# Kernel tuning notes

Hardware: AMD Instinct MI355X
Metric: run time of the kernel (lower is better)

## Reference

```python
import jax, jax.numpy as jnp
import numpy as np

N, E, F_IN = 100000, 600000, 128
HID, NCLS = 128, 2
# ratio=0.8 applied three times: ceil(0.8*100000), ceil(0.8*80000), ceil(0.8*64000)
K1, K2, K3 = 80000, 64000, 51200


def setup_inputs() -> dict:
    key = jax.random.key(0)
    k = jax.random.split(key, 16)
    s = 0.05
    p = {}
    p['x'] = jax.random.normal(k[0], (N, F_IN), dtype=jnp.float32)
    p['edge_index'] = jax.random.randint(k[1], (2, E), 0, N)
    # GraphConv i: out = lin_rel(sum_j x_j) + lin_root(x_i); lin_root has no bias (PyG)
    p['Wr1'] = jax.random.normal(k[2], (HID, F_IN), jnp.float32) * s
    p['br1'] = jnp.zeros((HID,), jnp.float32)
    p['Wroot1'] = jax.random.normal(k[3], (HID, F_IN), jnp.float32) * s
    p['pw1'] = jax.random.normal(k[4], (HID,), jnp.float32) * s
    p['Wr2'] = jax.random.normal(k[5], (HID, HID), jnp.float32) * s
    p['br2'] = jnp.zeros((HID,), jnp.float32)
    p['Wroot2'] = jax.random.normal(k[6], (HID, HID), jnp.float32) * s
    p['pw2'] = jax.random.normal(k[7], (HID,), jnp.float32) * s
    p['Wr3'] = jax.random.normal(k[8], (HID, HID), jnp.float32) * s
    p['br3'] = jnp.zeros((HID,), jnp.float32)
    p['Wroot3'] = jax.random.normal(k[9], (HID, HID), jnp.float32) * s
    p['pw3'] = jax.random.normal(k[10], (HID,), jnp.float32) * s
    p['W_lin1'] = jax.random.normal(k[11], (HID, 2 * HID), jnp.float32) * s
    p['b_lin1'] = jnp.zeros((HID,), jnp.float32)
    p['W_lin2'] = jax.random.normal(k[12], (64, HID), jnp.float32) * s
    p['b_lin2'] = jnp.zeros((64,), jnp.float32)
    p['W_lin3'] = jax.random.normal(k[13], (NCLS, 64), jnp.float32) * s
    p['b_lin3'] = jnp.zeros((NCLS,), jnp.float32)
    return p


def _gconv(x, src, dst, emask, Wr, br, Wroot):
    # PyG GraphConv(aggr='add'): masked edges contribute zero (== removed edge)
    msg = x[src] * emask[:, None].astype(x.dtype)           # [E, F]
    agg = jax.ops.segment_sum(msg, dst, num_segments=x.shape[0])
    return agg @ Wr.T + br + x @ Wroot.T


def _topk_pool(x, src, dst, emask, w, k):
    # PyG TopKPooling: score = tanh((x.w)/||w||); keep top-k nodes; x = x[perm]*score[perm]
    score = jnp.tanh((x @ w) / jnp.linalg.norm(w))
    vals, perm = jax.lax.top_k(score, k)
    x_new = x[perm] * vals[:, None]
    new_idx = jnp.full((x.shape[0],), -1, jnp.int32).at[perm].set(
        jnp.arange(k, dtype=jnp.int32))
    ns, nd = new_idx[src], new_idx[dst]
    valid = emask & (ns >= 0) & (nd >= 0)
    return x_new, jnp.where(valid, ns, 0), jnp.where(valid, nd, 0), valid


def _readout(x):
    # single graph (batch=None): gmp || gap -> [1, 2F]
    return jnp.concatenate([x.max(axis=0), x.mean(axis=0)])[None, :]


def reference(x, edge_index, Wr1, br1, Wroot1, pw1, Wr2, br2, Wroot2, pw2,
              Wr3, br3, Wroot3, pw3, W_lin1, b_lin1, W_lin2, b_lin2, W_lin3, b_lin3):
    src = edge_index[0].astype(jnp.int32)
    dst = edge_index[1].astype(jnp.int32)
    emask = jnp.ones((src.shape[0],), dtype=bool)

    h = jax.nn.relu(_gconv(x, src, dst, emask, Wr1, br1, Wroot1))
    h, src, dst, emask = _topk_pool(h, src, dst, emask, pw1, K1)
    r1 = _readout(h)

    h = jax.nn.relu(_gconv(h, src, dst, emask, Wr2, br2, Wroot2))
    h, src, dst, emask = _topk_pool(h, src, dst, emask, pw2, K2)
    r2 = _readout(h)

    h = jax.nn.relu(_gconv(h, src, dst, emask, Wr3, br3, Wroot3))
    h, src, dst, emask = _topk_pool(h, src, dst, emask, pw3, K3)
    r3 = _readout(h)

    z = r1 + r2 + r3                                        # [1, 256]
    z = jax.nn.relu(z @ W_lin1.T + b_lin1)                  # dropout: inference no-op
    z = jax.nn.relu(z @ W_lin2.T + b_lin2)
    return z @ W_lin3.T + b_lin3                            # [1, num_classes]
```

## Files before the change

kernel.cpp:

```cpp
#include <hip/hip_runtime.h>
#include <hip/hip_bf16.h>
#include <math.h>

#define N0 100000
#define E0 600000
#define KP1 80000
#define KP2 64000
#define KP3 51200
#define F 128
#define RPB 2048
#define RMID 128
#define SCAN_CHUNK 1024
#define NCHUNK ((N0 + SCAN_CHUNK - 1) / SCAN_CHUNK)

typedef __attribute__((ext_vector_type(8))) short short8;
typedef __attribute__((ext_vector_type(8))) unsigned short ushort8;
typedef __attribute__((ext_vector_type(4))) float f32x4;

__device__ __forceinline__ unsigned fkey(float f) {
    unsigned u = __float_as_uint(f);
    return u ^ ((u & 0x80000000u) ? 0xFFFFFFFFu : 0x80000000u);
}
__device__ __forceinline__ unsigned short f2b(float f) {
    __hip_bfloat16 h = __float2bfloat16(f);
    return *(unsigned short*)&h;
}
__device__ __forceinline__ float b2f(unsigned short u) {
    __hip_bfloat16 h;
    *(unsigned short*)&h = u;
    return __bfloat162float(h);
}

__global__ __launch_bounds__(256) void cvt4K(const float* __restrict__ in,
                                             unsigned short* __restrict__ out, int n4) {
    int i = blockIdx.x * 256 + threadIdx.x;
    if (i >= n4) return;
    float4 v = *(const float4*)(in + (size_t)i * 4);
    *(ushort4*)(out + (size_t)i * 4) = make_ushort4(f2b(v.x), f2b(v.y), f2b(v.z), f2b(v.w));
}

__global__ __launch_bounds__(256) void cvtWAllK(const float* __restrict__ a0, const float* __restrict__ a1,
                                                const float* __restrict__ a2, const float* __restrict__ a3,
                                                const float* __restrict__ a4, const float* __restrict__ a5,
                                                unsigned short* __restrict__ o) {
    int m = blockIdx.y;
    const float* src = (m == 0) ? a0 : (m == 1) ? a1 : (m == 2) ? a2 : (m == 3) ? a3 : (m == 4) ? a4 : a5;
    int i = blockIdx.x * 256 + threadIdx.x;
    float4 v = *(const float4*)(src + (size_t)i * 4);
    *(ushort4*)(o + (size_t)m * 16384 + (size_t)i * 4) = make_ushort4(f2b(v.x), f2b(v.y), f2b(v.z), f2b(v.w));
}

__global__ __launch_bounds__(128) void pwnK(const float* __restrict__ p0, const float* __restrict__ p1,
                                            const float* __restrict__ p2, float* __restrict__ pwn) {
    __shared__ float sh[128];
    int l = blockIdx.x, t = threadIdx.x;
    const float* p = (l == 0) ? p0 : (l == 1) ? p1 : p2;
    float v = p[t];
    sh[t] = v * v;
    __syncthreads();
    for (int off = 64; off; off >>= 1) {
        if (t < off) sh[t] += sh[t + off];
        __syncthreads();
    }
    pwn[l * 128 + t] = v / sqrtf(sh[0]);
}

__global__ __launch_bounds__(256) void histDstK(const int* __restrict__ dst, unsigned* __restrict__ cnt) {
    int e = blockIdx.x * 256 + threadIdx.x;
    if (e < E0) atomicAdd(&cnt[dst[e]], 1u);
}

__global__ __launch_bounds__(256) void scanReduceK(const unsigned* __restrict__ cnt,
                                                   unsigned* __restrict__ chunkSum, int nbins) {
    __shared__ unsigned sh[256];
    int base = blockIdx.x * SCAN_CHUNK + threadIdx.x * 4;
    unsigned s = 0;
#pragma unroll
    for (int i = 0; i < 4; i++) { int b = base + i; if (b < nbins) s += cnt[b]; }
    sh[threadIdx.x] = s;
    __syncthreads();
    for (int off = 128; off; off >>= 1) {
        if (threadIdx.x < off) sh[threadIdx.x] += sh[threadIdx.x + off];
        __syncthreads();
    }
    if (threadIdx.x == 0) chunkSum[blockIdx.x] = sh[0];
}

__global__ void scanChunksK(const unsigned* __restrict__ chunkSum, unsigned* __restrict__ chunkOff,
                            int nchunks, unsigned* __restrict__ totalOut) {
    if (threadIdx.x == 0) {
        unsigned run = 0;
        for (int i = 0; i < nchunks; i++) { chunkOff[i] = run; run += chunkSum[i]; }
        *totalOut = run;
    }
}

__global__ __launch_bounds__(256) void scanFinalK(const unsigned* __restrict__ cnt,
                                                  const unsigned* __restrict__ chunkOff,
                                                  unsigned* __restrict__ rowptr, int nbins) {
    __shared__ unsigned sh[256];
    int t = threadIdx.x;
    int base = blockIdx.x * SCAN_CHUNK + t * 4;
    unsigned c[4], s = 0;
#pragma unroll
    for (int i = 0; i < 4; i++) { int b = base + i; c[i] = (b < nbins) ? cnt[b] : 0u; s += c[i]; }
    sh[t] = s;
    __syncthreads();
    for (int off = 1; off < 256; off <<= 1) {
        unsigned v = (t >= off) ? sh[t - off] : 0u;
        __syncthreads();
        sh[t] += v;
        __syncthreads();
    }
    unsigned basep = chunkOff[blockIdx.x] + sh[t] - s;
#pragma unroll
    for (int i = 0; i < 4; i++) {
        int b = base + i;
        if (b < nbins) { rowptr[b] = basep; basep += c[i]; }
    }
}

__global__ __launch_bounds__(256) void scatterFillK(const int* __restrict__ src,
                                                    const int* __restrict__ dst,
                                                    const unsigned* __restrict__ rowptr,
                                                    unsigned* __restrict__ fill,
                                                    int* __restrict__ sortedSrc) {
    int e = blockIdx.x * 256 + threadIdx.x;
    if (e >= E0) return;
    int d = dst[e];
    unsigned p = rowptr[d] + atomicAdd(&fill[d], 1u);
    sortedSrc[p] = src[e];
}

__global__ __launch_bounds__(256) void iotaK(int* o, int n) {
    int i = blockIdx.x * 256 + threadIdx.x;
    if (i < n) o[i] = i;
}

__global__ __launch_bounds__(256) void aggSegB(const unsigned short* __restrict__ x,
                                               const int* __restrict__ srcCur,
                                               const unsigned* __restrict__ rowptr,
                                               const int* __restrict__ orig,
                                               unsigned short* __restrict__ agg, int n) {
    int g = blockIdx.x * 16 + (threadIdx.x >> 4);
    int q = threadIdx.x & 15;
    if (g >= n) return;
    int d = orig[g];
    unsigned e0 = rowptr[d], e1 = rowptr[d + 1];
    float a[8];
#pragma unroll
    for (int j = 0; j < 8; j++) a[j] = 0.f;
    unsigned e = e0;
    for (; e + 4 <= e1; e += 4) {
        int s0 = srcCur[e], s1 = srcCur[e + 1], s2 = srcCur[e + 2], s3 = srcCur[e + 3];
        ushort8 v0 = *(const ushort8*)(x + (size_t)(s0 < 0 ? 0 : s0) * F + q * 8);
        ushort8 v1 = *(const ushort8*)(x + (size_t)(s1 < 0 ? 0 : s1) * F + q * 8);
        ushort8 v2 = *(const ushort8*)(x + (size_t)(s2 < 0 ? 0 : s2) * F + q * 8);
        ushort8 v3 = *(const ushort8*)(x + (size_t)(s3 < 0 ? 0 : s3) * F + q * 8);
        float m0 = s0 < 0 ? 0.f : 1.f, m1 = s1 < 0 ? 0.f : 1.f;
        float m2 = s2 < 0 ? 0.f : 1.f, m3 = s3 < 0 ? 0.f : 1.f;
#pragma unroll
        for (int j = 0; j < 8; j++) {
            a[j] = fmaf(b2f(v0[j]), m0, a[j]);
            a[j] = fmaf(b2f(v1[j]), m1, a[j]);
            a[j] = fmaf(b2f(v2[j]), m2, a[j]);
            a[j] = fmaf(b2f(v3[j]), m3, a[j]);
        }
    }
    for (; e < e1; e++) {
        int s = srcCur[e];
        if (s < 0) continue;
        ushort8 v = *(const ushort8*)(x + (size_t)s * F + q * 8);
#pragma unroll
        for (int j = 0; j < 8; j++) a[j] += b2f(v[j]);
    }
    ushort8 o;
#pragma unroll
    for (int j = 0; j < 8; j++) o[j] = f2b(a[j]);
    *(ushort8*)(agg + (size_t)g * F + q * 8) = o;
}

__global__ __launch_bounds__(256) void buildOrigK(const int* __restrict__ origIn,
                                                  const int* __restrict__ nidx,
                                                  int* __restrict__ origOut, int n) {
    int i = blockIdx.x * 256 + threadIdx.x;
    if (i < n) { int ni = nidx[i]; if (ni >= 0) origOut[ni] = origIn[i]; }
}

__global__ __launch_bounds__(256) void remapSrcK(const int* __restrict__ srcIn,
                                                 const int* __restrict__ nidx,
                                                 int* __restrict__ srcOut) {
    int e = blockIdx.x * 256 + threadIdx.x;
    if (e >= E0) return;
    int s = srcIn[e];
    srcOut[e] = (s >= 0) ? nidx[s] : -1;
}

#define CPAD 40
__global__ __launch_bounds__(256) void convM(const unsigned short* __restrict__ A0,
                                             const unsigned short* __restrict__ A1,
                                             const unsigned short* __restrict__ W0,
                                             const unsigned short* __restrict__ W1,
                                             const float* __restrict__ br,
                                             const float* __restrict__ pwn,
                                             unsigned short* __restrict__ hbf,
                                             float* __restrict__ sc,
                                             unsigned* __restrict__ keys, int n) {
    __shared__ unsigned short As[128 * CPAD];
    __shared__ unsigned short Bs[128 * CPAD];
    int tid = threadIdx.x;
    int w = tid >> 6, l = tid & 63;
    int r = l & 15, g = l >> 4;
    int bm = blockIdx.x * 128;
    int srow = tid >> 2, q4 = tid & 3;

    f32x4 acc[2][8];
#pragma unroll
    for (int m = 0; m < 2; m++)
#pragma unroll
        for (int c = 0; c < 8; c++) acc[m][c] = (f32x4){0.f, 0.f, 0.f, 0.f};

    for (int ph = 0; ph < 2; ph++) {
        const unsigned short* A = ph ? A1 : A0;
        const unsigned short* W = ph ? W1 : W0;
        for (int kk = 0; kk < 128; kk += 32) {
            __syncthreads();
#pragma unroll
            for (int h2 = 0; h2 < 2; h2++) {
                int rr = srow + h2 * 64;
                uint4 av = make_uint4(0u, 0u, 0u, 0u);
                if (bm + rr < n) av = *(const uint4*)(A + (size_t)(bm + rr) * F + kk + q4 * 8);
                *(uint4*)(&As[rr * CPAD + q4 * 8]) = av;
                uint4 wv = *(const uint4*)(W + (size_t)rr * F + kk + q4 * 8);
                *(uint4*)(&Bs[rr * CPAD + q4 * 8]) = wv;
            }
            __syncthreads();
            short8 af[2], bf[8];
#pragma unroll
            for (int m = 0; m < 2; m++)
                af[m] = *(const short8*)(&As[(w * 32 + m * 16 + r) * CPAD + g * 8]);
#pragma unroll
            for (int c = 0; c < 8; c++)
                bf[c] = *(const short8*)(&Bs[(c * 16 + r) * CPAD + g * 8]);
#pragma unroll
            for (int m = 0; m < 2; m++)
#pragma unroll
                for (int c = 0; c < 8; c++)
                    acc[m][c] = __builtin_amdgcn_mfma_f32_16x16x32_bf16(af[m], bf[c], acc[m][c], 0, 0, 0);
        }
    }

    float pd[2][4];
#pragma unroll
    for (int m = 0; m < 2; m++)
#pragma unroll
        for (int j = 0; j < 4; j++) pd[m][j] = 0.f;

#pragma unroll
    for (int c = 0; c < 8; c++) {
        int col = c * 16 + r;
        float bias = br[col];
        float pwc = pwn[col];
#pragma unroll
        for (int m = 0; m < 2; m++) {
#pragma unroll
            for (int j = 0; j < 4; j++) {
                int row = bm + w * 32 + m * 16 + g * 4 + j;
                float h = fmaxf(acc[m][c][j] + bias, 0.f);
                pd[m][j] += h * pwc;
                if (row < n) hbf[(size_t)row * F + col] = f2b(h);
            }
        }
    }
#pragma unroll
    for (int m = 0; m < 2; m++) {
#pragma unroll
        for (int j = 0; j < 4; j++) {
            float p = pd[m][j];
            p += __shfl_xor(p, 1);
            p += __shfl_xor(p, 2);
            p += __shfl_xor(p, 4);
            p += __shfl_xor(p, 8);
            if (r == 0) {
                int row = bm + w * 32 + m * 16 + g * 4 + j;
                if (row < n) {
                    float s = tanhf(p);
                    sc[row] = s;
                    keys[row] = fkey(s);
                }
            }
        }
    }
}

__global__ void initSelK(unsigned* hist, unsigned* st, unsigned* done, unsigned* done2, int k) {
    hist[threadIdx.x] = 0;
    if (threadIdx.x == 0) { st[0] = 0u; st[1] = (unsigned)k; *done = 0u; *done2 = 0u; }
}

__global__ __launch_bounds__(256) void histSelK(const unsigned* __restrict__ keys, int n,
                                                int p, unsigned* __restrict__ st,
                                                unsigned* __restrict__ hist,
                                                unsigned* __restrict__ done, int nb) {
    __shared__ unsigned lh[256];
    __shared__ bool last;
    int tid = threadIdx.x;
    lh[tid] = 0;
    __syncthreads();
    unsigned prefix = st[0];
    int i = blockIdx.x * 256 + tid;
    if (i < n) {
        unsigned key = keys[i];
        bool m = (p == 0) || ((key >> (32 - 8 * p)) == (prefix >> (32 - 8 * p)));
        if (m) atomicAdd(&lh[(key >> (24 - 8 * p)) & 255u], 1u);
    }
    __syncthreads();
    if (lh[tid]) atomicAdd(&hist[tid], lh[tid]);
    __syncthreads();
    if (tid == 0) {
        __threadfence();
        last = (atomicAdd(done, 1u) == (unsigned)(nb - 1));
    }
    __syncthreads();
    if (!last) return;
    lh[tid] = atomicAdd(&hist[tid], 0u);
    __syncthreads();
    hist[tid] = 0;
    if (tid == 0) {
        unsigned krem = st[1], cum = 0;
        for (int b = 255; b >= 0; b--) {
            unsigned c = lh[b];
            if (cum + c >= krem) {
                st[0] |= ((unsigned)b) << (24 - 8 * p);
                st[1] = krem - cum;
                break;
            }
            cum += c;
        }
        *done = 0u;
    }
}

__global__ __launch_bounds__(256) void countsK(const unsigned* __restrict__ keys, int n,
                                               const unsigned* __restrict__ st,
                                               int* __restrict__ bGT, int* __restrict__ bEQ,
                                               int* __restrict__ sGT, int* __restrict__ sEQ,
                                               unsigned* __restrict__ done2, int nb) {
    __shared__ int cg_, ce_;
    __shared__ bool last;
    int tid = threadIdx.x;
    if (tid == 0) { cg_ = 0; ce_ = 0; }
    __syncthreads();
    unsigned t = st[0];
    int g = 0, e = 0;
    for (int it = 0; it < 4; it++) {
        int i = blockIdx.x * 1024 + it * 256 + tid;
        if (i < n) {
            unsigned k = keys[i];
            g += (k > t);
            e += (k == t);
        }
    }
    atomicAdd(&cg_, g);
    atomicAdd(&ce_, e);
    __syncthreads();
    if (tid == 0) {
        bGT[blockIdx.x] = cg_;
        bEQ[blockIdx.x] = ce_;
        __threadfence();
        last = (atomicAdd(done2, 1u) == (unsigned)(nb - 1));
    }
    __syncthreads();
    if (!last) return;
    if (tid == 0) {
        int gs = 0, es = 0;
        for (int b = 0; b < nb; b++) {
            sGT[b] = gs; sEQ[b] = es;
            gs += atomicAdd(&bGT[b], 0);
            es += atomicAdd(&bEQ[b], 0);
        }
        *done2 = 0u;
    }
}

__global__ __launch_bounds__(256) void markK(const unsigned* __restrict__ keys, int n,
                                             const unsigned* __restrict__ st,
                                             const int* __restrict__ sGT,
                                             const int* __restrict__ sEQ,
                                             int* __restrict__ nidx) {
    __shared__ int wG[4], wE[4];
    __shared__ int runG, runE;
    int tid = threadIdx.x, wv = tid >> 6, lane = tid & 63;
    if (tid == 0) { runG = 0; runE = 0; }
    unsigned t = st[0];
    int needEq = (int)st[1];
    int gOff = sGT[blockIdx.x], eOff = sEQ[blockIdx.x];
    unsigned long long mlt = (((unsigned long long)1) << lane) - 1ull;
    __syncthreads();
    for (int it = 0; it < 4; it++) {
        int i = blockIdx.x * 1024 + it * 256 + tid;
        bool inb = i < n;
        unsigned k = inb ? keys[i] : 0u;
        bool pG = inb && (k > t), pE = inb && (k == t);
        unsigned long long bG = __ballot(pG), bE = __ballot(pE);
        int lpG = __popcll(bG & mlt), lpE = __popcll(bE & mlt);
        if (lane == 0) { wG[wv] = __popcll(bG); wE[wv] = __popcll(bE); }
        __syncthreads();
        int woG = 0, woE = 0;
        for (int w = 0; w < wv; w++) { woG += wG[w]; woE += wE[w]; }
        int gB = gOff + runG + woG + lpG;
        int eB = eOff + runE + woE + lpE;
        int ni = -1;
        if (pG) ni = gB + (eB < needEq ? eB : needEq);
        else if (pE && eB < needEq) ni = gB + eB;
        if (inb) nidx[i] = ni;
        __syncthreads();
        if (tid == 0) {
            runG += wG[0] + wG[1] + wG[2] + wG[3];
            runE += wE[0] + wE[1] + wE[2] + wE[3];
        }
        __syncthreads();
    }
}

__global__ __launch_bounds__(256) void gatherB(const unsigned short* __restrict__ h,
                                               const float* __restrict__ sc,
                                               const int* __restrict__ nidx,
                                               unsigned short* __restrict__ out, int n) {
    int t = blockIdx.x * 256 + threadIdx.x;
    int i = t >> 4, q = t & 15;
    if (i >= n) return;
    int ni = nidx[i];
    if (ni < 0) return;
    float s = sc[i];
    ushort8 v = *(const ushort8*)(h + (size_t)i * F + q * 8);
    ushort8 o;
#pragma unroll
    for (int j = 0; j < 8; j++) o[j] = f2b(b2f(v[j]) * s);
    *(ushort8*)(out + (size_t)ni * F + q * 8) = o;
}

__global__ __launch_bounds__(128) void rpartK(const unsigned short* __restrict__ x, int k,
                                              float* __restrict__ pmax, float* __restrict__ psum) {
    int f = threadIdx.x;
    float m = -INFINITY, s = 0.f;
    for (int row = blockIdx.x; row < k; row += gridDim.x) {
        float v = b2f(x[(size_t)row * F + f]);
        m = fmaxf(m, v);
        s += v;
    }
    pmax[(size_t)blockIdx.x * F + f] = m;
    psum[(size_t)blockIdx.x * F + f] = s;
}

__global__ __launch_bounds__(128) void rmidK(const float* __restrict__ pmax,
                                             const float* __restrict__ psum,
                                             float* __restrict__ mmax,
                                             float* __restrict__ msum) {
    int f = threadIdx.x;
    int b0 = blockIdx.x * (RPB / RMID);
    float m = -INFINITY, s = 0.f;
#pragma unroll
    for (int i = 0; i < RPB / RMID; i++) {
        m = fmaxf(m, pmax[(size_t)(b0 + i) * F + f]);
        s += psum[(size_t)(b0 + i) * F + f];
    }
    mmax[(size_t)blockIdx.x * F + f] = m;
    msum[(size_t)blockIdx.x * F + f] = s;
}

__global__ __launch_bounds__(128) void rfinalK(const float* __restrict__ mmax,
                                               const float* __restrict__ msum, int k,
                                               float* __restrict__ r) {
    int f = threadIdx.x;
    float m = -INFINITY, s = 0.f;
    for (int b = 0; b < RMID; b++) {
        m = fmaxf(m, mmax[(size_t)b * F + f]);
        s += msum[(size_t)b * F + f];
    }
    r[f] += m;
    r[F + f] += s / (float)k;
}

__global__ __launch_bounds__(256) void mlpK(const float* __restrict__ r,
                                            const float* __restrict__ W1, const float* __restrict__ b1,
                                            const float* __restrict__ W2, const float* __restrict__ b2,
                                            const float* __restrict__ W3, const float* __restrict__ b3,
                                            float* __restrict__ out) {
    __shared__ float z0[256], z1[128], z2[64];
    int t = threadIdx.x;
    z0[t] = r[t];
    __syncthreads();
    if (t < 128) {
        float a = b1[t];
        for (int kk = 0; kk < 256; kk++) a = fmaf(W1[t * 256 + kk], z0[kk], a);
        z1[t] = fmaxf(a, 0.f);
    }
    __syncthreads();
    if (t < 64) {
        float a = b2[t];
        for (int kk = 0; kk < 128; kk++) a = fmaf(W2[t * 128 + kk], z1[kk], a);
        z2[t] = fmaxf(a, 0.f);
    }
    __syncthreads();
    if (t < 2) {
        float a = b3[t];
        for (int kk = 0; kk < 64; kk++) a = fmaf(W3[t * 64 + kk], z2[kk], a);
        out[t] = a;
    }
}

extern "C" void kernel_launch(void* const* d_in, const int* in_sizes, int n_in,
                              void* d_out, int out_size, void* d_ws, size_t ws_size,
                              hipStream_t stream) {
    const float* x = (const float*)d_in[0];
    const int* ei = (const int*)d_in[1];
    const float* Wr[3]    = { (const float*)d_in[2],  (const float*)d_in[6],  (const float*)d_in[10] };
    const float* br[3]    = { (const float*)d_in[3],  (const float*)d_in[7],  (const float*)d_in[11] };
    const float* Wroot[3] = { (const float*)d_in[4],  (const float*)d_in[8],  (const float*)d_in[12] };
    const float* pw[3]    = { (const float*)d_in[5],  (const float*)d_in[9],  (const float*)d_in[13] };
    const float* W1 = (const float*)d_in[14];
    const float* b1 = (const float*)d_in[15];
    const float* W2 = (const float*)d_in[16];
    const float* b2 = (const float*)d_in[17];
    const float* W3 = (const float*)d_in[18];
    const float* b3 = (const float*)d_in[19];
    float* out = (float*)d_out;
    char* w = (char*)d_ws;

    size_t o = 0;
    auto alc = [&](size_t bytes) { size_t r = o; o += (bytes + 255) & ~(size_t)255; return r; };
    unsigned short* hbf    = (unsigned short*)(w + alc((size_t)N0 * F * 2));
    unsigned short* xbf    = (unsigned short*)(w + alc((size_t)N0 * F * 2));
    unsigned short* aggbf  = (unsigned short*)(w + alc((size_t)N0 * F * 2));
    unsigned short* bufBbf = (unsigned short*)(w + alc((size_t)KP1 * F * 2));
    unsigned short* wbf    = (unsigned short*)(w + alc((size_t)6 * 16384 * 2));
    float*    pwn    = (float*)(w + alc(3 * 128 * 4));
    float*    sc     = (float*)(w + alc((size_t)N0 * 4));
    unsigned* keys   = (unsigned*)(w + alc((size_t)N0 * 4));
    int*      nidx   = (int*)(w + alc((size_t)N0 * 4));
    int*      sSrc0  = (int*)(w + alc((size_t)E0 * 4));
    int*      srcCA  = (int*)(w + alc((size_t)E0 * 4));
    int*      srcCB  = (int*)(w + alc((size_t)E0 * 4));
    unsigned* cnt    = (unsigned*)(w + alc((size_t)N0 * 4));
    unsigned* rowptr = (unsigned*)(w + alc((size_t)(N0 + 1) * 4));
    int*      origA  = (int*)(w + alc((size_t)N0 * 4));
    int*      origB  = (int*)(w + alc((size_t)N0 * 4));
    unsigned* chS    = (unsigned*)(w + alc(NCHUNK * 4));
    unsigned* chO    = (unsigned*)(w + alc(NCHUNK * 4));
    unsigned* hist   = (unsigned*)(w + alc(256 * 4));
    unsigned* st     = (unsigned*)(w + alc(64));
    unsigned* done   = (unsigned*)(w + alc(64));
    unsigned* done2  = (unsigned*)(w + alc(64));
    int*      bGT    = (int*)(w + alc(128 * 4));
    int*      bEQ    = (int*)(w + alc(128 * 4));
    int*      sGT    = (int*)(w + alc(128 * 4));
    int*      sEQ    = (int*)(w + alc(128 * 4));
    float*    r      = (float*)(w + alc(256 * 4));
    float*    pmax   = (float*)(w + alc((size_t)RPB * F * 4));
    float*    psum   = (float*)(w + alc((size_t)RPB * F * 4));
    float*    mmax   = (float*)(w + alc((size_t)RMID * F * 4));
    float*    msum   = (float*)(w + alc((size_t)RMID * F * 4));
    if (o > ws_size) return;

    const int* srcOrig = ei;
    const int* dstOrig = ei + E0;

    cvt4K<<<(N0 * F / 4 + 255) / 256, 256, 0, stream>>>(x, xbf, N0 * F / 4);
    cvtWAllK<<<dim3(16, 6), 256, 0, stream>>>(Wr[0], Wroot[0], Wr[1], Wroot[1], Wr[2], Wroot[2], wbf);
    pwnK<<<3, 128, 0, stream>>>(pw[0], pw[1], pw[2], pwn);

    hipMemsetAsync(cnt, 0, (size_t)N0 * 4, stream);
    histDstK<<<(E0 + 255) / 256, 256, 0, stream>>>(dstOrig, cnt);
    scanReduceK<<<NCHUNK, 256, 0, stream>>>(cnt, chS, N0);
    scanChunksK<<<1, 1, 0, stream>>>(chS, chO, NCHUNK, rowptr + N0);
    scanFinalK<<<NCHUNK, 256, 0, stream>>>(cnt, chO, rowptr, N0);
    hipMemsetAsync(cnt, 0, (size_t)N0 * 4, stream);
    scatterFillK<<<(E0 + 255) / 256, 256, 0, stream>>>(srcOrig, dstOrig, rowptr, cnt, sSrc0);
    iotaK<<<(N0 + 255) / 256, 256, 0, stream>>>(origA, N0);

    hipMemsetAsync(r, 0, 256 * 4, stream);

    const int ns[3] = { N0, KP1, KP2 };
    const int ks[3] = { KP1, KP2, KP3 };
    const int* srcCur[3] = { sSrc0, srcCA, srcCB };
    int* srcNext[3] = { srcCA, srcCB, nullptr };
    const int* origCur[3] = { origA, origB, origA };
    int* origNext[3] = { origB, origA, nullptr };

    for (int L = 0; L < 3; L++) {
        int n = ns[L], k = ks[L];
        const unsigned short* xinbf = (L == 0) ? xbf : bufBbf;

        aggSegB<<<(n + 15) / 16, 256, 0, stream>>>(xinbf, srcCur[L], rowptr, origCur[L], aggbf, n);
        convM<<<(n + 127) / 128, 256, 0, stream>>>(aggbf, xinbf,
                                                   wbf + (size_t)(L * 2) * 16384,
                                                   wbf + (size_t)(L * 2 + 1) * 16384,
                                                   br[L], pwn + L * 128, hbf, sc, keys, n);

        initSelK<<<1, 256, 0, stream>>>(hist, st, done, done2, k);
        int nbh = (n + 255) / 256;
        for (int p = 0; p < 4; p++)
            histSelK<<<nbh, 256, 0, stream>>>(keys, n, p, st, hist, done, nbh);
        int nb = (n + 1023) / 1024;
        countsK<<<nb, 256, 0, stream>>>(keys, n, st, bGT, bEQ, sGT, sEQ, done2, nb);
        markK<<<nb, 256, 0, stream>>>(keys, n, st, sGT, sEQ, nidx);

        gatherB<<<(n * 16 + 255) / 256, 256, 0, stream>>>(hbf, sc, nidx, bufBbf, n);
        if (L < 2) {
            buildOrigK<<<(n + 255) / 256, 256, 0, stream>>>(origCur[L], nidx, origNext[L], n);
            remapSrcK<<<(E0 + 255) / 256, 256, 0, stream>>>(srcCur[L], nidx, srcNext[L]);
        }

        rpartK<<<RPB, 128, 0, stream>>>(bufBbf, k, pmax, psum);
        rmidK<<<RMID, 128, 0, stream>>>(pmax, psum, mmax, msum);
        rfinalK<<<1, 128, 0, stream>>>(mmax, msum, k, r);
    }

    mlpK<<<1, 256, 0, stream>>>(r, W1, b1, W2, b2, W3, b3, out);
}
```

Measured before the change: 640.1 us.

## Fuse CSR build and top-k selection chains into persistent kernels with grid barriers

Replaces the multi-launch CSR construction (memset, histogram, three scan kernels, scatter, iota) with one cooperative kernel that uses a software grid barrier. It does the same for the per-layer top-k pipeline: radix selection, counts, mark, gather-scale, orig/src remap and readout reduction all run in one kernel per layer. The aim is to remove many small kernel launches and memsets, plus the separate multi-stage readout reductions. The spin-wait grid barrier assumes every block is resident at once, which holds only because the grid is small (about 100 blocks), and it adds atomic polling on the critical path.

Result: slower. 961.2 us (+50.2%).

```diff
diff --git a/kernel.cpp b/kernel.cpp
--- a/kernel.cpp
+++ b/kernel.cpp
@@ -9,7 +9,6 @@
 #define KP3 51200
 #define F 128
 #define RPB 2048
-#define RMID 128
 #define SCAN_CHUNK 1024
 #define NCHUNK ((N0 + SCAN_CHUNK - 1) / SCAN_CHUNK)
 
@@ -31,8 +30,24 @@
     return __bfloat162float(h);
 }
 
+__device__ __forceinline__ void gbar(unsigned* bar, unsigned target) {
+    __threadfence();
+    __syncthreads();
+    if (threadIdx.x == 0) {
+        atomicAdd(bar, 1u);
+        while (atomicAdd(bar, 0u) < target) __builtin_amdgcn_s_sleep(1);
+        __threadfence();
+    }
+    __syncthreads();
+}
+
 __global__ __launch_bounds__(256) void cvt4K(const float* __restrict__ in,
-                                             unsigned short* __restrict__ out, int n4) {
+                                             unsigned short* __restrict__ out, int n4,
+                                             unsigned* __restrict__ bar, unsigned* __restrict__ hist) {
+    if (blockIdx.x == 0) {
+        if (threadIdx.x < 16) bar[threadIdx.x] = 0u;
+        hist[threadIdx.x] = 0u;
+    }
     int i = blockIdx.x * 256 + threadIdx.x;
     if (i >= n4) return;
     float4 v = *(const float4*)(in + (size_t)i * 4);
@@ -65,76 +80,65 @@
     pwn[l * 128 + t] = v / sqrtf(sh[0]);
 }
 
-__global__ __launch_bounds__(256) void histDstK(const int* __restrict__ dst, unsigned* __restrict__ cnt) {
-    int e = blockIdx.x * 256 + threadIdx.x;
-    if (e < E0) atomicAdd(&cnt[dst[e]], 1u);
-}
-
-__global__ __launch_bounds__(256) void scanReduceK(const unsigned* __restrict__ cnt,
-                                                   unsigned* __restrict__ chunkSum, int nbins) {
+__global__ __launch_bounds__(256) void csrK(const int* __restrict__ src, const int* __restrict__ dst,
+                                            unsigned* __restrict__ cnt, unsigned* __restrict__ rowptr,
+                                            int* __restrict__ orig, int* __restrict__ sortedSrc,
+                                            unsigned* __restrict__ chS, unsigned* __restrict__ chO,
+                                            unsigned* __restrict__ bar) {
     __shared__ unsigned sh[256];
-    int base = blockIdx.x * SCAN_CHUNK + threadIdx.x * 4;
-    unsigned s = 0;
-#pragma unroll
-    for (int i = 0; i < 4; i++) { int b = base + i; if (b < nbins) s += cnt[b]; }
-    sh[threadIdx.x] = s;
-    __syncthreads();
-    for (int off = 128; off; off >>= 1) {
-        if (threadIdx.x < off) sh[threadIdx.x] += sh[threadIdx.x + off];
+    int tid = threadIdx.x, b = blockIdx.x;
+    const unsigned NB = NCHUNK;
+    unsigned gen = 0;
+    for (int i = b * 256 + tid; i < N0; i += NCHUNK * 256) { cnt[i] = 0u; orig[i] = i; }
+    gen++; gbar(bar, gen * NB);
+    for (int e = b * 256 + tid; e < E0; e += NCHUNK * 256) atomicAdd(&cnt[dst[e]], 1u);
+    gen++; gbar(bar, gen * NB);
+    {
+        unsigned s = 0;
+        int base = b * SCAN_CHUNK + tid * 4;
+#pragma unroll
+        for (int j = 0; j < 4; j++) { int bin = base + j; if (bin < N0) s += atomicAdd(&cnt[bin], 0u); }
+        sh[tid] = s;
         __syncthreads();
-    }
-    if (threadIdx.x == 0) chunkSum[blockIdx.x] = sh[0];
-}
-
-__global__ void scanChunksK(const unsigned* __restrict__ chunkSum, unsigned* __restrict__ chunkOff,
-                            int nchunks, unsigned* __restrict__ totalOut) {
-    if (threadIdx.x == 0) {
+        for (int off = 128; off; off >>= 1) {
+            if (tid < off) sh[tid] += sh[tid + off];
+            __syncthreads();
+        }
+        if (tid == 0) atomicExch(&chS[b], sh[0]);
+    }
+    gen++; gbar(bar, gen * NB);
+    if (b == 0 && tid == 0) {
         unsigned run = 0;
-        for (int i = 0; i < nchunks; i++) { chunkOff[i] = run; run += chunkSum[i]; }
-        *totalOut = run;
-    }
-}
-
-__global__ __launch_bounds__(256) void scanFinalK(const unsigned* __restrict__ cnt,
-                                                  const unsigned* __restrict__ chunkOff,
-                                                  unsigned* __restrict__ rowptr, int nbins) {
-    __shared__ unsigned sh[256];
-    int t = threadIdx.x;
-    int base = blockIdx.x * SCAN_CHUNK + t * 4;
-    unsigned c[4], s = 0;
-#pragma unroll
-    for (int i = 0; i < 4; i++) { int b = base + i; c[i] = (b < nbins) ? cnt[b] : 0u; s += c[i]; }
-    sh[t] = s;
-    __syncthreads();
-    for (int off = 1; off < 256; off <<= 1) {
-        unsigned v = (t >= off) ? sh[t - off] : 0u;
+        for (int c = 0; c < NCHUNK; c++) { atomicExch(&chO[c], run); run += atomicAdd(&chS[c], 0u); }
+        rowptr[N0] = run;
+    }
+    gen++; gbar(bar, gen * NB);
+    {
+        int base = b * SCAN_CHUNK + tid * 4;
+        unsigned c[4], s = 0;
+#pragma unroll
+        for (int j = 0; j < 4; j++) { int bin = base + j; c[j] = (bin < N0) ? atomicAdd(&cnt[bin], 0u) : 0u; s += c[j]; }
+        sh[tid] = s;
         __syncthreads();
-        sh[t] += v;
-        __syncthreads();
-    }
-    unsigned basep = chunkOff[blockIdx.x] + sh[t] - s;
-#pragma unroll
-    for (int i = 0; i < 4; i++) {
-        int b = base + i;
-        if (b < nbins) { rowptr[b] = basep; basep += c[i]; }
-    }
-}
-
-__global__ __launch_bounds__(256) void scatterFillK(const int* __restrict__ src,
-                                                    const int* __restrict__ dst,
-                                                    const unsigned* __restrict__ rowptr,
-                                                    unsigned* __restrict__ fill,
-                                                    int* __restrict__ sortedSrc) {
-    int e = blockIdx.x * 256 + threadIdx.x;
-    if (e >= E0) return;
-    int d = dst[e];
-    unsigned p = rowptr[d] + atomicAdd(&fill[d], 1u);
-    sortedSrc[p] = src[e];
-}
-
-__global__ __launch_bounds__(256) void iotaK(int* o, int n) {
-    int i = blockIdx.x * 256 + threadIdx.x;
-    if (i < n) o[i] = i;
+        for (int off = 1; off < 256; off <<= 1) {
+            unsigned v = (tid >= off) ? sh[tid - off] : 0u;
+            __syncthreads();
+            sh[tid] += v;
+            __syncthreads();
+        }
+        unsigned basep = atomicAdd(&chO[b], 0u) + sh[tid] - s;
+#pragma unroll
+        for (int j = 0; j < 4; j++) {
+            int bin = base + j;
+            if (bin < N0) { rowptr[bin] = basep; basep += c[j]; cnt[bin] = 0u; }
+        }
+    }
+    gen++; gbar(bar, gen * NB);
+    for (int e = b * 256 + tid; e < E0; e += NCHUNK * 256) {
+        int d = dst[e];
+        unsigned p = rowptr[d] + atomicAdd(&cnt[d], 1u);
+        sortedSrc[p] = src[e];
+    }
 }
 
 __global__ __launch_bounds__(256) void aggSegB(const unsigned short* __restrict__ x,
@@ -178,22 +182,6 @@
 #pragma unroll
     for (int j = 0; j < 8; j++) o[j] = f2b(a[j]);
     *(ushort8*)(agg + (size_t)g * F + q * 8) = o;
-}
-
-__global__ __launch_bounds__(256) void buildOrigK(const int* __restrict__ origIn,
-                                                  const int* __restrict__ nidx,
-                                                  int* __restrict__ origOut, int n) {
-    int i = blockIdx.x * 256 + threadIdx.x;
-    if (i < n) { int ni = nidx[i]; if (ni >= 0) origOut[ni] = origIn[i]; }
-}
-
-__global__ __launch_bounds__(256) void remapSrcK(const int* __restrict__ srcIn,
-                                                 const int* __restrict__ nidx,
-                                                 int* __restrict__ srcOut) {
-    int e = blockIdx.x * 256 + threadIdx.x;
-    if (e >= E0) return;
-    int s = srcIn[e];
-    srcOut[e] = (s >= 0) ? nidx[s] : -1;
 }
 
 #define CPAD 40
@@ -293,193 +281,204 @@
     }
 }
 
-__global__ void initSelK(unsigned* hist, unsigned* st, unsigned* done, unsigned* done2, int k) {
-    hist[threadIdx.x] = 0;
-    if (threadIdx.x == 0) { st[0] = 0u; st[1] = (unsigned)k; *done = 0u; *done2 = 0u; }
-}
-
-__global__ __launch_bounds__(256) void histSelK(const unsigned* __restrict__ keys, int n,
-                                                int p, unsigned* __restrict__ st,
-                                                unsigned* __restrict__ hist,
-                                                unsigned* __restrict__ done, int nb) {
+__global__ __launch_bounds__(256) void selectAllK(
+    const unsigned* __restrict__ keys, const float* __restrict__ sc,
+    const unsigned short* __restrict__ hbf,
+    const int* __restrict__ origIn, int* __restrict__ origOut,
+    const int* __restrict__ srcIn, int* __restrict__ srcOut,
+    unsigned short* __restrict__ bufB,
+    float* __restrict__ pmax, float* __restrict__ psum,
+    float* __restrict__ r,
+    unsigned* __restrict__ bar, unsigned* __restrict__ hist,
+    unsigned* __restrict__ st,
+    unsigned* __restrict__ bGT, unsigned* __restrict__ bEQ,
+    unsigned* __restrict__ sGT, unsigned* __restrict__ sEQ,
+    int* __restrict__ nidx,
+    int n, int k, int nb, int doNext, int initR) {
     __shared__ unsigned lh[256];
-    __shared__ bool last;
-    int tid = threadIdx.x;
-    lh[tid] = 0;
-    __syncthreads();
-    unsigned prefix = st[0];
-    int i = blockIdx.x * 256 + tid;
-    if (i < n) {
-        unsigned key = keys[i];
-        bool m = (p == 0) || ((key >> (32 - 8 * p)) == (prefix >> (32 - 8 * p)));
-        if (m) atomicAdd(&lh[(key >> (24 - 8 * p)) & 255u], 1u);
-    }
-    __syncthreads();
-    if (lh[tid]) atomicAdd(&hist[tid], lh[tid]);
-    __syncthreads();
+    __shared__ unsigned shPfx, shKrem;
+    __shared__ int cg_, ce_;
+    __shared__ int wG[4], wE[4];
+    __shared__ int shG, shE, shRunG, shRunE;
+    __shared__ float redm[256 * 8];
+    __shared__ float reds[256 * 8];
+
+    int tid = threadIdx.x, b = blockIdx.x;
+    const unsigned NB = (unsigned)nb;
+    unsigned gen = 0;
+    unsigned pfx = 0, krem = (unsigned)k;
+
+    for (int p = 0; p < 4; p++) {
+        if (tid == 0) shPfx = (p == 0) ? 0u : atomicAdd(&st[0], 0u);
+        lh[tid] = 0;
+        __syncthreads();
+        unsigned prefix = shPfx;
+        int sh = 32 - 8 * p;
+#pragma unroll
+        for (int it = 0; it < 4; it++) {
+            int i = b * 1024 + it * 256 + tid;
+            if (i < n) {
+                unsigned key = keys[i];
+                bool m = (p == 0) || ((key >> sh) == (prefix >> sh));
+                if (m) atomicAdd(&lh[(key >> (24 - 8 * p)) & 255u], 1u);
+            }
+        }
+        __syncthreads();
+        if (lh[tid]) atomicAdd(&hist[tid], lh[tid]);
+        gen++; gbar(bar, gen * NB);
+        if (b == 0) {
+            lh[tid] = atomicExch(&hist[tid], 0u);
+            __syncthreads();
+            if (tid == 0) {
+                unsigned cum = 0;
+                for (int bin = 255; bin >= 0; bin--) {
+                    unsigned cc = lh[bin];
+                    if (cum + cc >= krem) {
+                        pfx |= ((unsigned)bin) << (24 - 8 * p);
+                        krem -= cum;
+                        break;
+                    }
+                    cum += cc;
+                }
+                atomicExch(&st[0], pfx);
+                atomicExch(&st[1], krem);
+            }
+            __syncthreads();
+        }
+        gen++; gbar(bar, gen * NB);
+    }
+
+    if (tid == 0) { shPfx = atomicAdd(&st[0], 0u); shKrem = atomicAdd(&st[1], 0u); }
+    __syncthreads();
+    unsigned thr = shPfx;
+    int needEq = (int)shKrem;
+
+    if (tid == 0) { cg_ = 0; ce_ = 0; }
+    __syncthreads();
+    {
+        int g2 = 0, e2 = 0;
+#pragma unroll
+        for (int it = 0; it < 4; it++) {
+            int i = b * 1024 + it * 256 + tid;
+            if (i < n) {
+                unsigned kk = keys[i];
+                g2 += (kk > thr);
+                e2 += (kk == thr);
+            }
+        }
+        atomicAdd(&cg_, g2);
+        atomicAdd(&ce_, e2);
+    }
+    __syncthreads();
+    if (tid == 0) { atomicExch(&bGT[b], (unsigned)cg_); atomicExch(&bEQ[b], (unsigned)ce_); }
+    gen++; gbar(bar, gen * NB);
+    if (b == 0 && tid == 0) {
+        unsigned gs = 0, es = 0;
+        for (int bb = 0; bb < nb; bb++) {
+            atomicExch(&sGT[bb], gs);
+            atomicExch(&sEQ[bb], es);
+            gs += atomicAdd(&bGT[bb], 0u);
+            es += atomicAdd(&bEQ[bb], 0u);
+        }
+    }
+    gen++; gbar(bar, gen * NB);
+
     if (tid == 0) {
-        __threadfence();
-        last = (atomicAdd(done, 1u) == (unsigned)(nb - 1));
-    }
-    __syncthreads();
-    if (!last) return;
-    lh[tid] = atomicAdd(&hist[tid], 0u);
-    __syncthreads();
-    hist[tid] = 0;
-    if (tid == 0) {
-        unsigned krem = st[1], cum = 0;
-        for (int b = 255; b >= 0; b--) {
-            unsigned c = lh[b];
-            if (cum + c >= krem) {
-                st[0] |= ((unsigned)b) << (24 - 8 * p);
-                st[1] = krem - cum;
-                break;
-            }
-            cum += c;
-        }
-        *done = 0u;
-    }
-}
-
-__global__ __launch_bounds__(256) void countsK(const unsigned* __restrict__ keys, int n,
-                                               const unsigned* __restrict__ st,
-                                               int* __restrict__ bGT, int* __restrict__ bEQ,
-                                               int* __restrict__ sGT, int* __restrict__ sEQ,
-                                               unsigned* __restrict__ done2, int nb) {
-    __shared__ int cg_, ce_;
-    __shared__ bool last;
-    int tid = threadIdx.x;
-    if (tid == 0) { cg_ = 0; ce_ = 0; }
-    __syncthreads();
-    unsigned t = st[0];
-    int g = 0, e = 0;
-    for (int it = 0; it < 4; it++) {
-        int i = blockIdx.x * 1024 + it * 256 + tid;
-        if (i < n) {
-            unsigned k = keys[i];
-            g += (k > t);
-            e += (k == t);
-        }
-    }
-    atomicAdd(&cg_, g);
-    atomicAdd(&ce_, e);
-    __syncthreads();
-    if (tid == 0) {
-        bGT[blockIdx.x] = cg_;
-        bEQ[blockIdx.x] = ce_;
-        __threadfence();
-        last = (atomicAdd(done2, 1u) == (unsigned)(nb - 1));
-    }
-    __syncthreads();
-    if (!last) return;
-    if (tid == 0) {
-        int gs = 0, es = 0;
-        for (int b = 0; b < nb; b++) {
-            sGT[b] = gs; sEQ[b] = es;
-            gs += atomicAdd(&bGT[b], 0);
-            es += atomicAdd(&bEQ[b], 0);
-        }
-        *done2 = 0u;
-    }
-}
-
-__global__ __launch_bounds__(256) void markK(const unsigned* __restrict__ keys, int n,
-                                             const unsigned* __restrict__ st,
-                                             const int* __restrict__ sGT,
-                                             const int* __restrict__ sEQ,
-                                             int* __restrict__ nidx) {
-    __shared__ int wG[4], wE[4];
-    __shared__ int runG, runE;
-    int tid = threadIdx.x, wv = tid >> 6, lane = tid & 63;
-    if (tid == 0) { runG = 0; runE = 0; }
-    unsigned t = st[0];
-    int needEq = (int)st[1];
-    int gOff = sGT[blockIdx.x], eOff = sEQ[blockIdx.x];
-    unsigned long long mlt = (((unsigned long long)1) << lane) - 1ull;
-    __syncthreads();
-    for (int it = 0; it < 4; it++) {
-        int i = blockIdx.x * 1024 + it * 256 + tid;
-        bool inb = i < n;
-        unsigned k = inb ? keys[i] : 0u;
-        bool pG = inb && (k > t), pE = inb && (k == t);
-        unsigned long long bG = __ballot(pG), bE = __ballot(pE);
-        int lpG = __popcll(bG & mlt), lpE = __popcll(bE & mlt);
-        if (lane == 0) { wG[wv] = __popcll(bG); wE[wv] = __popcll(bE); }
+        shG = (int)atomicAdd(&sGT[b], 0u);
+        shE = (int)atomicAdd(&sEQ[b], 0u);
+        shRunG = 0; shRunE = 0;
+    }
+    __syncthreads();
+    {
+        int gOff = shG, eOff = shE;
+        int wv = tid >> 6, lane = tid & 63;
+        unsigned long long mlt = (((unsigned long long)1) << lane) - 1ull;
+        for (int it = 0; it < 4; it++) {
+            int i = b * 1024 + it * 256 + tid;
+            bool inb = i < n;
+            unsigned kk = inb ? keys[i] : 0u;
+            bool pG = inb && (kk > thr), pE = inb && (kk == thr);
+            unsigned long long bG = __ballot(pG), bE = __ballot(pE);
+            int lpG = __popcll(bG & mlt), lpE = __popcll(bE & mlt);
+            if (lane == 0) { wG[wv] = __popcll(bG); wE[wv] = __popcll(bE); }
+            __syncthreads();
+            int woG = 0, woE = 0;
+            for (int w2 = 0; w2 < wv; w2++) { woG += wG[w2]; woE += wE[w2]; }
+            int gB = gOff + shRunG + woG + lpG;
+            int eB = eOff + shRunE + woE + lpE;
+            int ni = -1;
+            if (pG) ni = gB + (eB < needEq ? eB : needEq);
+            else if (pE && eB < needEq) ni = gB + eB;
+            if (inb) {
+                nidx[i] = ni;
+                if (doNext && ni >= 0) origOut[ni] = origIn[i];
+            }
+            __syncthreads();
+            if (tid == 0) {
+                shRunG += wG[0] + wG[1] + wG[2] + wG[3];
+                shRunE += wE[0] + wE[1] + wE[2] + wE[3];
+            }
+            __syncthreads();
+        }
+    }
+    gen++; gbar(bar, gen * NB);
+
+    {
+        int q = tid & 15;
+        float lm[8], ls[8];
+#pragma unroll
+        for (int j = 0; j < 8; j++) { lm[j] = -INFINITY; ls[j] = 0.f; }
+        for (int t = b * 256 + tid; t < n * 16; t += nb * 256) {
+            int i = t >> 4;
+            int ni = nidx[i];
+            if (ni < 0) continue;
+            float s = sc[i];
+            ushort8 v = *(const ushort8*)(hbf + (size_t)i * F + q * 8);
+            ushort8 o;
+#pragma unroll
+            for (int j = 0; j < 8; j++) {
+                o[j] = f2b(b2f(v[j]) * s);
+                float fb = b2f(o[j]);
+                lm[j] = fmaxf(lm[j], fb);
+                ls[j] += fb;
+            }
+            *(ushort8*)(bufB + (size_t)ni * F + q * 8) = o;
+        }
+        if (doNext) {
+            for (int e2 = b * 256 + tid; e2 < E0; e2 += nb * 256) {
+                int s2 = srcIn[e2];
+                srcOut[e2] = (s2 >= 0) ? nidx[s2] : -1;
+            }
+        }
+#pragma unroll
+        for (int j = 0; j < 8; j++) { redm[tid * 8 + j] = lm[j]; reds[tid * 8 + j] = ls[j]; }
         __syncthreads();
-        int woG = 0, woE = 0;
-        for (int w = 0; w < wv; w++) { woG += wG[w]; woE += wE[w]; }
-        int gB = gOff + runG + woG + lpG;
-        int eB = eOff + runE + woE + lpE;
-        int ni = -1;
-        if (pG) ni = gB + (eB < needEq ? eB : needEq);
-        else if (pE && eB < needEq) ni = gB + eB;
-        if (inb) nidx[i] = ni;
-        __syncthreads();
-        if (tid == 0) {
-            runG += wG[0] + wG[1] + wG[2] + wG[3];
-            runE += wE[0] + wE[1] + wE[2] + wE[3];
-        }
-        __syncthreads();
-    }
-}
-
-__global__ __launch_bounds__(256) void gatherB(const unsigned short* __restrict__ h,
-                                               const float* __restrict__ sc,
-                                               const int* __restrict__ nidx,
-                                               unsigned short* __restrict__ out, int n) {
-    int t = blockIdx.x * 256 + threadIdx.x;
-    int i = t >> 4, q = t & 15;
-    if (i >= n) return;
-    int ni = nidx[i];
-    if (ni < 0) return;
-    float s = sc[i];
-    ushort8 v = *(const ushort8*)(h + (size_t)i * F + q * 8);
-    ushort8 o;
-#pragma unroll
-    for (int j = 0; j < 8; j++) o[j] = f2b(b2f(v[j]) * s);
-    *(ushort8*)(out + (size_t)ni * F + q * 8) = o;
-}
-
-__global__ __launch_bounds__(128) void rpartK(const unsigned short* __restrict__ x, int k,
-                                              float* __restrict__ pmax, float* __restrict__ psum) {
-    int f = threadIdx.x;
-    float m = -INFINITY, s = 0.f;
-    for (int row = blockIdx.x; row < k; row += gridDim.x) {
-        float v = b2f(x[(size_t)row * F + f]);
-        m = fmaxf(m, v);
-        s += v;
-    }
-    pmax[(size_t)blockIdx.x * F + f] = m;
-    psum[(size_t)blockIdx.x * F + f] = s;
-}
-
-__global__ __launch_bounds__(128) void rmidK(const float* __restrict__ pmax,
-                                             const float* __restrict__ psum,
-                                             float* __restrict__ mmax,
-                                             float* __restrict__ msum) {
-    int f = threadIdx.x;
-    int b0 = blockIdx.x * (RPB / RMID);
-    float m = -INFINITY, s = 0.f;
-#pragma unroll
-    for (int i = 0; i < RPB / RMID; i++) {
-        m = fmaxf(m, pmax[(size_t)(b0 + i) * F + f]);
-        s += psum[(size_t)(b0 + i) * F + f];
-    }
-    mmax[(size_t)blockIdx.x * F + f] = m;
-    msum[(size_t)blockIdx.x * F + f] = s;
-}
-
-__global__ __launch_bounds__(128) void rfinalK(const float* __restrict__ mmax,
-                                               const float* __restrict__ msum, int k,
-                                               float* __restrict__ r) {
-    int f = threadIdx.x;
-    float m = -INFINITY, s = 0.f;
-    for (int b = 0; b < RMID; b++) {
-        m = fmaxf(m, mmax[(size_t)b * F + f]);
-        s += msum[(size_t)b * F + f];
-    }
-    r[f] += m;
-    r[F + f] += s / (float)k;
+        if (tid < 16) {
+            for (int g2 = 1; g2 < 16; g2++) {
+#pragma unroll
+                for (int j = 0; j < 8; j++) {
+                    lm[j] = fmaxf(lm[j], redm[(g2 * 16 + tid) * 8 + j]);
+                    ls[j] += reds[(g2 * 16 + tid) * 8 + j];
+                }
+            }
+#pragma unroll
+            for (int j = 0; j < 8; j++) {
+                pmax[b * 128 + tid * 8 + j] = lm[j];
+                psum[b * 128 + tid * 8 + j] = ls[j];
+            }
+        }
+    }
+    gen++; gbar(bar, gen * NB);
+
+    if (b == 0 && tid < 128) {
+        float m = -INFINITY, s = 0.f;
+        for (int bb = 0; bb < nb; bb++) {
+            m = fmaxf(m, pmax[bb * 128 + tid]);
+            s += psum[bb * 128 + tid];
+        }
+        if (initR) { r[tid] = m; r[128 + tid] = s / (float)k; }
+        else       { r[tid] += m; r[128 + tid] += s / (float)k; }
+    }
 }
 
 __global__ __launch_bounds__(256) void mlpK(const float* __restrict__ r,
@@ -550,43 +549,31 @@
     unsigned* chO    = (unsigned*)(w + alc(NCHUNK * 4));
     unsigned* hist   = (unsigned*)(w + alc(256 * 4));
     unsigned* st     = (unsigned*)(w + alc(64));
-    unsigned* done   = (unsigned*)(w + alc(64));
-    unsigned* done2  = (unsigned*)(w + alc(64));
-    int*      bGT    = (int*)(w + alc(128 * 4));
-    int*      bEQ    = (int*)(w + alc(128 * 4));
-    int*      sGT    = (int*)(w + alc(128 * 4));
-    int*      sEQ    = (int*)(w + alc(128 * 4));
+    unsigned* barA   = (unsigned*)(w + alc(16 * 4));
+    unsigned* bGT    = (unsigned*)(w + alc(128 * 4));
+    unsigned* bEQ    = (unsigned*)(w + alc(128 * 4));
+    unsigned* sGT    = (unsigned*)(w + alc(128 * 4));
+    unsigned* sEQ    = (unsigned*)(w + alc(128 * 4));
     float*    r      = (float*)(w + alc(256 * 4));
     float*    pmax   = (float*)(w + alc((size_t)RPB * F * 4));
     float*    psum   = (float*)(w + alc((size_t)RPB * F * 4));
-    float*    mmax   = (float*)(w + alc((size_t)RMID * F * 4));
-    float*    msum   = (float*)(w + alc((size_t)RMID * F * 4));
     if (o > ws_size) return;
 
     const int* srcOrig = ei;
     const int* dstOrig = ei + E0;
 
-    cvt4K<<<(N0 * F / 4 + 255) / 256, 256, 0, stream>>>(x, xbf, N0 * F / 4);
+    cvt4K<<<(N0 * F / 4 + 255) / 256, 256, 0, stream>>>(x, xbf, N0 * F / 4, barA, hist);
     cvtWAllK<<<dim3(16, 6), 256, 0, stream>>>(Wr[0], Wroot[0], Wr[1], Wroot[1], Wr[2], Wroot[2], wbf);
     pwnK<<<3, 128, 0, stream>>>(pw[0], pw[1], pw[2], pwn);
 
-    hipMemsetAsync(cnt, 0, (size_t)N0 * 4, stream);
-    histDstK<<<(E0 + 255) / 256, 256, 0, stream>>>(dstOrig, cnt);
-    scanReduceK<<<NCHUNK, 256, 0, stream>>>(cnt, chS, N0);
-    scanChunksK<<<1, 1, 0, stream>>>(chS, chO, NCHUNK, rowptr + N0);
-    scanFinalK<<<NCHUNK, 256, 0, stream>>>(cnt, chO, rowptr, N0);
-    hipMemsetAsync(cnt, 0, (size_t)N0 * 4, stream);
-    scatterFillK<<<(E0 + 255) / 256, 256, 0, stream>>>(srcOrig, dstOrig, rowptr, cnt, sSrc0);
-    iotaK<<<(N0 + 255) / 256, 256, 0, stream>>>(origA, N0);
-
-    hipMemsetAsync(r, 0, 256 * 4, stream);
+    csrK<<<NCHUNK, 256, 0, stream>>>(srcOrig, dstOrig, cnt, rowptr, origA, sSrc0, chS, chO, barA + 3);
 
     const int ns[3] = { N0, KP1, KP2 };
     const int ks[3] = { KP1, KP2, KP3 };
     const int* srcCur[3] = { sSrc0, srcCA, srcCB };
-    int* srcNext[3] = { srcCA, srcCB, nullptr };
+    int* srcNext[3] = { srcCA, srcCB, srcCA };
     const int* origCur[3] = { origA, origB, origA };
-    int* origNext[3] = { origB, origA, nullptr };
+    int* origNext[3] = { origB, origA, origB };
 
     for (int L = 0; L < 3; L++) {
         int n = ns[L], k = ks[L];
@@ -597,24 +584,12 @@
                                                    wbf + (size_t)(L * 2) * 16384,
                                                    wbf + (size_t)(L * 2 + 1) * 16384,
                                                    br[L], pwn + L * 128, hbf, sc, keys, n);
-
-        initSelK<<<1, 256, 0, stream>>>(hist, st, done, done2, k);
-        int nbh = (n + 255) / 256;
-        for (int p = 0; p < 4; p++)
-            histSelK<<<nbh, 256, 0, stream>>>(keys, n, p, st, hist, done, nbh);
         int nb = (n + 1023) / 1024;
-        countsK<<<nb, 256, 0, stream>>>(keys, n, st, bGT, bEQ, sGT, sEQ, done2, nb);
-        markK<<<nb, 256, 0, stream>>>(keys, n, st, sGT, sEQ, nidx);
-
-        gatherB<<<(n * 16 + 255) / 256, 256, 0, stream>>>(hbf, sc, nidx, bufBbf, n);
-        if (L < 2) {
-            buildOrigK<<<(n + 255) / 256, 256, 0, stream>>>(origCur[L], nidx, origNext[L], n);
-            remapSrcK<<<(E0 + 255) / 256, 256, 0, stream>>>(srcCur[L], nidx, srcNext[L]);
-        }
-
-        rpartK<<<RPB, 128, 0, stream>>>(bufBbf, k, pmax, psum);
-        rmidK<<<RMID, 128, 0, stream>>>(pmax, psum, mmax, msum);
-        rfinalK<<<1, 128, 0, stream>>>(mmax, msum, k, r);
+        selectAllK<<<nb, 256, 0, stream>>>(keys, sc, hbf,
+                                           origCur[L], origNext[L], srcCur[L], srcNext[L],
+                                           bufBbf, pmax, psum, r,
+                                           barA + L, hist, st, bGT, bEQ, sGT, sEQ, nidx,
+                                           n, k, nb, (L < 2) ? 1 : 0, (L == 0) ? 1 : 0);
     }
 
     mlpK<<<1, 256, 0, stream>>>(r, W1, b1, W2, b2, W3, b3, out);
```
